# Kernel optimization log

Measured on AMD Instinct MI355X. Metric: run time of the kernel, lower is better.

Reference implementation:

```python
import jax, jax.numpy as jnp
import numpy as np

HID, NH, HD, MD = 512, 8, 64, 16  # hidden_dim, num_heads, head_dim, manifold_dim
B, S = 4, 1024
FLOW_STEPS, DT = 10, 0.1
EPS = 1e-8


def _cplx_weight(k, shape, std=0.02):
    kr, ki = jax.random.split(k)
    w = jax.random.normal(kr, shape) + 1j * jax.random.normal(ki, shape)
    return (w * std).astype(jnp.complex64)


def setup_inputs() -> dict:
    key = jax.random.key(0)
    ks = jax.random.split(key, 12)
    inp = {}
    inp['x_real'] = jax.random.normal(ks[0], (B, S, HID), dtype=jnp.float32)
    inp['x_imag'] = jax.random.normal(ks[1], (B, S, HID), dtype=jnp.float32)
    # manifold projection head_dim -> manifold_dim
    inp['Wm'] = _cplx_weight(ks[2], (MD, HD), std=HD ** -0.5)
    inp['bm'] = jnp.zeros((MD,), jnp.complex64)
    inp['Wq'] = _cplx_weight(ks[3], (MD, MD))
    inp['bq'] = jnp.zeros((MD,), jnp.complex64)
    inp['Wk'] = _cplx_weight(ks[4], (MD, MD))
    inp['bk'] = jnp.zeros((MD,), jnp.complex64)
    inp['Wv'] = _cplx_weight(ks[5], (MD, MD))
    inp['bv'] = jnp.zeros((MD,), jnp.complex64)
    # learned manifold metric (initialized to identity as in the module)
    inp['metric'] = jnp.eye(MD, dtype=jnp.complex64)
    # output projection expanded_dim = NH*MD -> hidden_dim
    inp['Wo'] = _cplx_weight(ks[6], (HID, NH * MD))
    inp['bo'] = jnp.zeros((HID,), jnp.complex64)
    return inp


def _forward(x_real, x_imag, Wm, bm, Wq, bq, Wk, bk, Wv, bv, metric, Wo, bo):
    x = (x_real + 1j * x_imag).astype(jnp.complex64)            # [B,S,HID]
    b, s, _ = x.shape
    h = x.reshape(b, s, NH, HD).transpose(0, 2, 1, 3)           # [B,NH,S,HD]
    # project onto low-dim manifold coordinates
    m = h @ Wm.T + bm                                           # [B,NH,S,MD]
    # hyperbolic exponential map at origin (curvature -1): tanh(|v|)/|v| * v
    n = jnp.sqrt(jnp.sum(jnp.abs(m) ** 2, -1, keepdims=True)) + EPS
    m = (jnp.tanh(n) / n) * m
    # parallel transport via the learned metric
    m = m @ metric
    # geometric flow: 10 Euler integration steps with dt=0.1
    sym = 0.5 * (metric + metric.conj().T)

    def step(carry, _):
        vel = carry @ sym - carry
        return carry + DT * vel, None

    m, _ = jax.lax.scan(step, m, None, length=FLOW_STEPS)
    # hyperbolic logarithm map at origin: artanh(|u|)/|u| * u
    n2 = jnp.sqrt(jnp.sum(jnp.abs(m) ** 2, -1, keepdims=True))
    n2 = jnp.clip(n2, EPS, 1.0 - 1e-6)
    m = (jnp.arctanh(n2) / n2) * m
    # complex q/k/v attention on manifold coordinates
    q = m @ Wq.T + bq
    k = m @ Wk.T + bk
    v = m @ Wv.T + bv
    scale = HD ** -0.5  # module uses self.scale = head_dim ** -0.5
    scores = jnp.einsum('bhsd,bhtd->bhst', q, jnp.conj(k)).real * scale  # [B,NH,S,S]
    attn = jax.nn.softmax(scores, axis=-1).astype(jnp.complex64)
    out = jnp.einsum('bhst,bhtd->bhsd', attn, v)                # [B,NH,S,MD]
    expanded = out.transpose(0, 2, 1, 3).reshape(b, s, NH * MD)  # [B,S,NH*MD]
    return expanded @ Wo.T + bo + x                              # residual, [B,S,HID]


def reference(x_real, x_imag, Wm, bm, Wq, bq, Wk, bk, Wv, bv, metric, Wo, bo):
    return _forward(x_real, x_imag, Wm, bm, Wq, bq, Wk, bk, Wv, bv, metric, Wo, bo)
```

## Files before the change

### kernel.cpp

```cpp
#include <hip/hip_runtime.h>
#include <math.h>

#define HIDD 512
#define NHH 8
#define HDD 64
#define MDD 16
#define Bz 4
#define Sz 1024
#define DTf 0.1f
#define EPSf 1e-8f
#define SCALEf 0.125f

typedef unsigned short ushort_t;
typedef unsigned int uint_t;

typedef __attribute__((ext_vector_type(8))) short bf16x8;
typedef __attribute__((ext_vector_type(4))) float f32x4;

constexpr size_t OFF_QB   = 0;
constexpr size_t OFF_KB   = OFF_QB + 262144;
constexpr size_t OFF_VT   = OFF_KB + 262144;
constexpr size_t OFF_E    = OFF_VT + 262144;
constexpr size_t OFF_WOT  = OFF_E + (size_t)Bz * Sz * NHH * MDD;

__device__ __forceinline__ float bf2f(ushort_t u) {
  union { unsigned int i; float f; } c;
  c.i = ((unsigned int)u) << 16;
  return c.f;
}
__device__ __forceinline__ ushort_t f2bf(float f) {
  unsigned int x = __float_as_uint(f);
  unsigned int r = (x + 0x7fffu + ((x >> 16) & 1u)) >> 16;
  return (ushort_t)r;
}
__device__ __forceinline__ float2 ldc(const void* p, int i, bool bf) {
  if (bf) {
    ushort2 u = ((const ushort2*)p)[i];
    return make_float2(bf2f(u.x), bf2f(u.y));
  }
  return ((const float2*)p)[i];
}
__device__ __forceinline__ float ldr(const void* p, size_t i, bool bf) {
  if (bf) return bf2f(((const ushort_t*)p)[i]);
  return ((const float*)p)[i];
}
__device__ __forceinline__ float2 cmadd(float2 acc, float2 a, float2 b) {
  acc.x = fmaf(a.x, b.x, fmaf(-a.y, b.y, acc.x));
  acc.y = fmaf(a.x, b.y, fmaf(a.y, b.x, acc.y));
  return acc;
}

__global__ __launch_bounds__(256) void k_qkv(
    const void* __restrict__ xr, const void* __restrict__ xi,
    const void* __restrict__ Wm, const void* __restrict__ bm,
    const void* __restrict__ Wq, const void* __restrict__ bq,
    const void* __restrict__ Wk, const void* __restrict__ bk,
    const void* __restrict__ Wv, const void* __restrict__ bv,
    const void* __restrict__ metric,
    ushort_t* __restrict__ Qb, ushort_t* __restrict__ Kb,
    ushort_t* __restrict__ VTb) {
  __shared__ float2 hs[64 * 65];
  __shared__ float2 msc[64 * 17];
  __shared__ float2 wmt[64 * 16];
  __shared__ float2 Tm[256];
  __shared__ float2 wqt[256], wkt[256], wvt[256];
  __shared__ float2 bms[16], bqs[16], bks[16], bvs[16];
  __shared__ int votes[4];
  float2* msc2 = hs;

  int tid = threadIdx.x;
  int bh = blockIdx.y;
  int s0 = blockIdx.x * 64;

  const uint_t* mu = (const uint_t*)metric;
  bool cbf = (mu[0] == 0x00003F80u);
  int ti = tid >> 4, tj = tid & 15;

  {
    unsigned e = (((const ushort_t*)xr)[tid] >> 7) & 0xFFu;
    unsigned long long bal = __ballot(e >= 100u && e <= 134u);
    if ((tid & 63) == 0) votes[tid >> 6] = (int)__popcll(bal);
  }

  wqt[tid] = ldc(metric, tid, cbf);
  #pragma unroll
  for (int it = 0; it < 4; it++) {
    int c = tid + it * 256;
    int d = c >> 6, e = c & 63;
    wmt[e * 16 + d] = ldc(Wm, c, cbf);
  }
  float2 wq_r = ldc(Wq, tid, cbf);
  float2 wk_r = ldc(Wk, tid, cbf);
  float2 wv_r = ldc(Wv, tid, cbf);
  float2 bm_r = make_float2(0.f, 0.f), bq_r = bm_r, bk_r = bm_r, bv_r = bm_r;
  if (tid < 16) {
    bm_r = ldc(bm, tid, cbf); bq_r = ldc(bq, tid, cbf);
    bk_r = ldc(bk, tid, cbf); bv_r = ldc(bv, tid, cbf);
  }
  __syncthreads();
  bool xbf = (votes[0] + votes[1] + votes[2] + votes[3]) > 192;

  size_t xoff = ((size_t)(((bh >> 3) * Sz) + s0)) * HIDD + (bh & 7) * HDD;
  ushort4 xur[4], xui[4];
  float4 xfr[4], xfi[4];
  if (xbf) {
    const ushort_t* xrb = (const ushort_t*)xr + xoff;
    const ushort_t* xib = (const ushort_t*)xi + xoff;
    #pragma unroll
    for (int it = 0; it < 4; it++) {
      int idx = tid + it * 256;
      int i = idx >> 4, e4 = idx & 15;
      xur[it] = ((const ushort4*)(xrb + (size_t)i * HIDD))[e4];
      xui[it] = ((const ushort4*)(xib + (size_t)i * HIDD))[e4];
    }
  } else {
    const float* xrb = (const float*)xr + xoff;
    const float* xib = (const float*)xi + xoff;
    #pragma unroll
    for (int it = 0; it < 4; it++) {
      int idx = tid + it * 256;
      int i = idx >> 4, e4 = idx & 15;
      xfr[it] = ((const float4*)(xrb + (size_t)i * HIDD))[e4];
      xfi[it] = ((const float4*)(xib + (size_t)i * HIDD))[e4];
    }
  }

  #define MATMUL16(DST, S1, S2)                                              \
    {                                                                        \
      float2 acc_ = make_float2(0.f, 0.f);                                   \
      _Pragma("unroll")                                                      \
      for (int k_ = 0; k_ < 16; k_++)                                        \
        acc_ = cmadd(acc_, S1[ti * 16 + k_], S2[k_ * 16 + tj]);              \
      DST[tid] = acc_;                                                       \
    }
  {
    float2 a = wqt[tid];
    float2 bt = wqt[tj * 16 + ti];
    float2 symv = make_float2(0.5f * (a.x + bt.x), 0.5f * (a.y - bt.y));
    float2 Mv = make_float2(DTf * symv.x, DTf * symv.y);
    if (ti == tj) Mv.x += 1.0f - DTf;
    wkt[tid] = Mv;
  }
  __syncthreads();
  MATMUL16(wvt, wkt, wkt);
  __syncthreads();
  MATMUL16(Tm, wvt, wvt);
  __syncthreads();
  MATMUL16(wvt, Tm, wkt);
  __syncthreads();
  MATMUL16(Tm, wvt, wvt);
  __syncthreads();
  float2 Tacc = make_float2(0.f, 0.f);
  #pragma unroll
  for (int k = 0; k < 16; k++) Tacc = cmadd(Tacc, wqt[ti * 16 + k], Tm[k * 16 + tj]);
  __syncthreads();
  #undef MATMUL16

  Tm[tid] = Tacc;
  wqt[tj * 16 + ti] = wq_r;
  wkt[tj * 16 + ti] = wk_r;
  wvt[tj * 16 + ti] = wv_r;
  if (tid < 16) { bms[tid] = bm_r; bqs[tid] = bq_r; bks[tid] = bk_r; bvs[tid] = bv_r; }
  if (xbf) {
    #pragma unroll
    for (int it = 0; it < 4; it++) {
      int idx = tid + it * 256;
      int i = idx >> 4, e = (idx & 15) * 4;
      hs[i * 65 + e + 0] = make_float2(bf2f(xur[it].x), bf2f(xui[it].x));
      hs[i * 65 + e + 1] = make_float2(bf2f(xur[it].y), bf2f(xui[it].y));
      hs[i * 65 + e + 2] = make_float2(bf2f(xur[it].z), bf2f(xui[it].z));
      hs[i * 65 + e + 3] = make_float2(bf2f(xur[it].w), bf2f(xui[it].w));
    }
  } else {
    #pragma unroll
    for (int it = 0; it < 4; it++) {
      int idx = tid + it * 256;
      int i = idx >> 4, e = (idx & 15) * 4;
      hs[i * 65 + e + 0] = make_float2(xfr[it].x, xfi[it].x);
      hs[i * 65 + e + 1] = make_float2(xfr[it].y, xfi[it].y);
      hs[i * 65 + e + 2] = make_float2(xfr[it].z, xfi[it].z);
      hs[i * 65 + e + 3] = make_float2(xfr[it].w, xfi[it].w);
    }
  }
  __syncthreads();

  int tok = tid >> 2, g = tid & 3;
  int jb = g * 4;

  float2 acc[4];
  #pragma unroll
  for (int i2 = 0; i2 < 4; i2++) acc[i2] = bms[jb + i2];
  for (int e = 0; e < 64; e++) {
    float2 hv = hs[tok * 65 + e];
    #pragma unroll
    for (int i2 = 0; i2 < 4; i2++) acc[i2] = cmadd(acc[i2], hv, wmt[e * 16 + jb + i2]);
  }
  float nn = 0.f;
  #pragma unroll
  for (int i2 = 0; i2 < 4; i2++) nn += acc[i2].x * acc[i2].x + acc[i2].y * acc[i2].y;
  nn += __shfl_xor(nn, 1);
  nn += __shfl_xor(nn, 2);
  float n1 = sqrtf(nn) + EPSf;
  float te = __expf(2.f * n1);
  float sc1 = (te - 1.f) / ((te + 1.f) * n1);
  #pragma unroll
  for (int i2 = 0; i2 < 4; i2++)
    msc[tok * 17 + jb + i2] = make_float2(acc[i2].x * sc1, acc[i2].y * sc1);
  __syncthreads();

  float2 m2[4];
  #pragma unroll
  for (int i2 = 0; i2 < 4; i2++) m2[i2] = make_float2(0.f, 0.f);
  for (int d = 0; d < 16; d++) {
    float2 mv = msc[tok * 17 + d];
    #pragma unroll
    for (int i2 = 0; i2 < 4; i2++) m2[i2] = cmadd(m2[i2], mv, Tm[d * 16 + jb + i2]);
  }
  float nn2 = 0.f;
  #pragma unroll
  for (int i2 = 0; i2 < 4; i2++) nn2 += m2[i2].x * m2[i2].x + m2[i2].y * m2[i2].y;
  nn2 += __shfl_xor(nn2, 1);
  nn2 += __shfl_xor(nn2, 2);
  float n2 = sqrtf(nn2);
  n2 = fminf(fmaxf(n2, EPSf), 1.0f - 1e-6f);
  float fac = 0.5f * __logf((1.f + n2) / (1.f - n2)) / n2;
  #pragma unroll
  for (int i2 = 0; i2 < 4; i2++)
    msc2[tok * 17 + jb + i2] = make_float2(m2[i2].x * fac, m2[i2].y * fac);
  __syncthreads();

  float2 qa[4], ka[4], va[4];
  #pragma unroll
  for (int i2 = 0; i2 < 4; i2++) { qa[i2] = bqs[jb + i2]; ka[i2] = bks[jb + i2]; va[i2] = bvs[jb + i2]; }
  for (int d = 0; d < 16; d++) {
    float2 mv = msc2[tok * 17 + d];
    #pragma unroll
    for (int i2 = 0; i2 < 4; i2++) {
      qa[i2] = cmadd(qa[i2], mv, wqt[d * 16 + jb + i2]);
      ka[i2] = cmadd(ka[i2], mv, wkt[d * 16 + jb + i2]);
      va[i2] = cmadd(va[i2], mv, wvt[d * 16 + jb + i2]);
    }
  }
  int s = s0 + tok;
  uint_t qp[4], kp[4];
  #pragma unroll
  for (int i2 = 0; i2 < 4; i2++) {
    qp[i2] = (uint_t)f2bf(qa[i2].x * SCALEf) | ((uint_t)f2bf(qa[i2].y * SCALEf) << 16);
    kp[i2] = (uint_t)f2bf(ka[i2].x) | ((uint_t)f2bf(ka[i2].y) << 16);
  }
  size_t rowbase = ((size_t)bh * Sz + s) * 32 + (size_t)g * 8;
  *(uint4*)(Qb + rowbase) = make_uint4(qp[0], qp[1], qp[2], qp[3]);
  *(uint4*)(Kb + rowbase) = make_uint4(kp[0], kp[1], kp[2], kp[3]);
  size_t vtb = (size_t)bh * 32 * Sz;
  #pragma unroll
  for (int i2 = 0; i2 < 4; i2++) {
    int d = (jb + i2) * 2;
    VTb[vtb + (size_t)d * Sz + s]       = f2bf(va[i2].x);
    VTb[vtb + (size_t)(d + 1) * Sz + s] = f2bf(va[i2].y);
  }
}

__global__ __launch_bounds__(256) void k_attn_mf(const ushort_t* __restrict__ Qb,
                                                 const ushort_t* __restrict__ Kb,
                                                 const ushort_t* __restrict__ VTb,
                                                 float* __restrict__ ef,
                                                 const void* __restrict__ Wo,
                                                 float2* __restrict__ WoT,
                                                 ushort_t* __restrict__ Ab,
                                                 ushort_t* __restrict__ Bb,
                                                 const void* __restrict__ metric,
                                                 int cmode) {
  __shared__ ushort_t Ks[128 * 88];
  __shared__ ushort_t VTs[32 * 152];
  __shared__ ushort_t Ps[4 * 16 * 136];
  int tid = threadIdx.x;

  {
    bool cbf = (((const uint_t*)metric)[0] == 0x00003F80u);
    if (tid < 128) {
      int idx = (blockIdx.y * 16 + blockIdx.x) * 128 + tid;
      float2 wv = ldc(Wo, idx, cbf);
      if (cmode) {
        int o = idx >> 7, j = idx & 127;
        WoT[(size_t)j * 512 + o] = wv;
      } else {
        ((ushort2*)Bb)[idx] = make_ushort2(f2bf(wv.x), f2bf(-wv.y));
      }
    }
  }

  int w = tid >> 6, lane = tid & 63;
  int n = lane & 15, qd = lane >> 4;
  int bh = blockIdx.y;
  int qb = blockIdx.x * 64 + w * 16;

  const ushort_t* Qh = Qb + (size_t)bh * Sz * 32;
  const ushort_t* Kh = Kb + (size_t)bh * Sz * 32;
  const ushort_t* VTh = VTb + (size_t)bh * 32 * Sz;

  bf16x8 qf = *(const bf16x8*)(Qh + (size_t)(qb + n) * 32 + qd * 8);

  f32x4 o0 = {0.f, 0.f, 0.f, 0.f}, o1 = {0.f, 0.f, 0.f, 0.f};
  float m_run = 0.f, l_run = 0.f;
  ushort_t* Pw = Ps + w * 16 * 136;

  for (int kc = 0; kc < Sz; kc += 128) {
    __syncthreads();
    {
      int row = tid >> 1, half = tid & 1;
      const uint4* sk = (const uint4*)(Kh + (size_t)(kc + row) * 32 + half * 16);
      uint4 a = sk[0], b2 = sk[1];
      *(uint4*)(Ks + row * 88 + half * 16) = a;
      *(uint4*)(Ks + row * 88 + half * 16 + 8) = b2;
      int d = tid >> 3, seg = tid & 7;
      const uint4* sv = (const uint4*)(VTh + (size_t)d * Sz + kc + seg * 16);
      uint4 c = sv[0], e2 = sv[1];
      *(uint4*)(VTs + d * 152 + seg * 16) = c;
      *(uint4*)(VTs + d * 152 + seg * 16 + 8) = e2;
    }
    __syncthreads();

    f32x4 st[8];
    __builtin_amdgcn_s_setprio(1);
    #pragma unroll
    for (int s = 0; s < 4; s++) {
      bf16x8 ka0 = *(const bf16x8*)(Ks + (s * 32 + n) * 88 + qd * 8);
      bf16x8 ka1 = *(const bf16x8*)(Ks + (s * 32 + 16 + n) * 88 + qd * 8);
      f32x4 z = {0.f, 0.f, 0.f, 0.f};
      st[2 * s]     = __builtin_amdgcn_mfma_f32_16x16x32_bf16(ka0, qf, z, 0, 0, 0);
      st[2 * s + 1] = __builtin_amdgcn_mfma_f32_16x16x32_bf16(ka1, qf, z, 0, 0, 0);
    }
    __builtin_amdgcn_s_setprio(0);

    float mt = st[0][0];
    #pragma unroll
    for (int i = 0; i < 8; i++) {
      #pragma unroll
      for (int r = 0; r < 4; r++) mt = fmaxf(mt, st[i][r]);
    }
    mt = fmaxf(mt, __shfl_xor(mt, 16));
    mt = fmaxf(mt, __shfl_xor(mt, 32));
    if (!__all(mt - m_run <= 8.f)) {
      float mnew = fmaxf(m_run, mt);
      float alpha = __expf(m_run - mnew);
      l_run *= alpha;
      float ar0 = __shfl(alpha, qd * 4 + 0);
      float ar1 = __shfl(alpha, qd * 4 + 1);
      float ar2 = __shfl(alpha, qd * 4 + 2);
      float ar3 = __shfl(alpha, qd * 4 + 3);
      o0[0] *= ar0; o0[1] *= ar1; o0[2] *= ar2; o0[3] *= ar3;
      o1[0] *= ar0; o1[1] *= ar1; o1[2] *= ar2; o1[3] *= ar3;
      m_run = mnew;
    }

    float lt = 0.f;
    #pragma unroll
    for (int s = 0; s < 4; s++) {
      float p0[4], p1[4];
      #pragma unroll
      for (int r = 0; r < 4; r++) {
        p0[r] = __expf(st[2 * s][r] - m_run);
        p1[r] = __expf(st[2 * s + 1][r] - m_run);
        lt += p0[r] + p1[r];
      }
      uint2 w0, w1;
      w0.x = (uint_t)f2bf(p0[0]) | ((uint_t)f2bf(p0[1]) << 16);
      w0.y = (uint_t)f2bf(p0[2]) | ((uint_t)f2bf(p0[3]) << 16);
      w1.x = (uint_t)f2bf(p1[0]) | ((uint_t)f2bf(p1[1]) << 16);
      w1.y = (uint_t)f2bf(p1[2]) | ((uint_t)f2bf(p1[3]) << 16);
      *(uint2*)(Pw + n * 136 + s * 32 + qd * 4) = w0;
      *(uint2*)(Pw + n * 136 + s * 32 + 16 + qd * 4) = w1;
    }
    l_run += lt;

    __builtin_amdgcn_s_setprio(1);
    #pragma unroll
    for (int s = 0; s < 4; s++) {
      bf16x8 pa  = *(const bf16x8*)(Pw + n * 136 + s * 32 + qd * 8);
      bf16x8 vb0 = *(const bf16x8*)(VTs + n * 152 + s * 32 + qd * 8);
      bf16x8 vb1 = *(const bf16x8*)(VTs + (n + 16) * 152 + s * 32 + qd * 8);
      o0 = __builtin_amdgcn_mfma_f32_16x16x32_bf16(pa, vb0, o0, 0, 0, 0);
      o1 = __builtin_amdgcn_mfma_f32_16x16x32_bf16(pa, vb1, o1, 0, 0, 0);
    }
    __builtin_amdgcn_s_setprio(0);
  }

  l_run += __shfl_xor(l_run, 16);
  l_run += __shfl_xor(l_run, 32);
  int b = bh >> 3, h = bh & 7;
  if (cmode == 0) {
    #pragma unroll
    for (int r = 0; r < 4; r++) {
      float li = __shfl(l_run, qd * 4 + r);
      float inv = 1.0f / li;
      size_t gt = (size_t)(b * Sz + qb + qd * 4 + r);
      Ab[gt * 256 + h * 32 + n]      = f2bf(o0[r] * inv);
      Ab[gt * 256 + h * 32 + 16 + n] = f2bf(o1[r] * inv);
    }
  } else {
    #pragma unroll
    for (int r = 0; r < 4; r++) {
      float li = __shfl(l_run, qd * 4 + r);
      float inv = 1.0f / li;
      int tok = qb + qd * 4 + r;
      float* ep = ef + (((size_t)(b * Sz + tok)) * NHH + h) * 32;
      ep[n]      = o0[r] * inv;
      ep[16 + n] = o1[r] * inv;
    }
  }
}

__global__ __launch_bounds__(256) void k_proj_mf(const ushort_t* __restrict__ Ab,
                                                 const ushort_t* __restrict__ Bb,
                                                 const void* __restrict__ bo,
                                                 const void* __restrict__ xr,
                                                 const void* __restrict__ metric,
                                                 float* __restrict__ out) {
  __shared__ int votes[4];
  int tid = threadIdx.x;
  bool cbf = (((const uint_t*)metric)[0] == 0x00003F80u);
  {
    unsigned e = (((const ushort_t*)xr)[tid] >> 7) & 0xFFu;
    unsigned long long bal = __ballot(e >= 100u && e <= 134u);
    if ((tid & 63) == 0) votes[tid >> 6] = (int)__popcll(bal);
  }
  __syncthreads();
  bool xbf = (votes[0] + votes[1] + votes[2] + votes[3]) > 192;

  int w = tid >> 6, lane = tid & 63;
  int n = lane & 15, qd = lane >> 4;
  int tb = blockIdx.x * 16;
  int ob = blockIdx.y * 256 + w * 64;

  bf16x8 af[8];
  const ushort_t* Ar = Ab + (size_t)(tb + n) * 256 + qd * 8;
  #pragma unroll
  for (int ks = 0; ks < 8; ks++) af[ks] = *(const bf16x8*)(Ar + ks * 32);

  #pragma unroll
  for (int nt = 0; nt < 4; nt++) {
    int o = ob + nt * 16 + n;
    const ushort_t* Br = Bb + (size_t)o * 256 + qd * 8;
    f32x4 c = {0.f, 0.f, 0.f, 0.f};
    #pragma unroll
    for (int ks = 0; ks < 8; ks++) {
      bf16x8 bfr = *(const bf16x8*)(Br + ks * 32);
      c = __builtin_amdgcn_mfma_f32_16x16x32_bf16(bfr, af[ks], c, 0, 0, 0);
    }
    float bor = ldc(bo, o, cbf).x;
    #pragma unroll
    for (int r = 0; r < 4; r++) {
      size_t gt = (size_t)(tb + qd * 4 + r);
      out[gt * HIDD + o] = c[r] + bor + ldr(xr, gt * HIDD + o, xbf);
    }
  }
}

__global__ __launch_bounds__(256) void k_proj_c(const float2* __restrict__ ew,
                                                const float2* __restrict__ WoT,
                                                const void* __restrict__ bo,
                                                const void* __restrict__ xr,
                                                const void* __restrict__ xi,
                                                const void* __restrict__ metric,
                                                ushort2* __restrict__ out) {
  __shared__ float2 es[8 * 128];
  __shared__ int votes[4];
  int tid = threadIdx.x;
  bool cbf = (((const uint_t*)metric)[0] == 0x00003F80u);
  {
    unsigned e = (((const ushort_t*)xr)[tid] >> 7) & 0xFFu;
    unsigned long long bal = __ballot(e >= 100u && e <= 134u);
    if ((tid & 63) == 0) votes[tid >> 6] = (int)__popcll(bal);
  }
  int tok0 = blockIdx.x * 8;
  #pragma unroll
  for (int it = 0; it < 4; it++) {
    int idx = tid + it * 256;
    es[idx] = ew[(size_t)tok0 * 128 + idx];
  }
  __syncthreads();
  bool xbf = (votes[0] + votes[1] + votes[2] + votes[3]) > 192;
  for (int rep = 0; rep < 2; rep++) {
    int o = tid + rep * 256;
    float2 accT[8];
    #pragma unroll
    for (int t = 0; t < 8; t++) accT[t] = make_float2(0.f, 0.f);
    #pragma unroll 2
    for (int j = 0; j < 128; j++) {
      float2 wv = WoT[(size_t)j * 512 + o];
      #pragma unroll
      for (int t = 0; t < 8; t++) accT[t] = cmadd(accT[t], es[t * 128 + j], wv);
    }
    float2 bov = ldc(bo, o, cbf);
    #pragma unroll
    for (int t = 0; t < 8; t++) {
      size_t gt = tok0 + t;
      float rx = accT[t].x + bov.x + ldr(xr, gt * HIDD + o, xbf);
      float ry = accT[t].y + bov.y + ldr(xi, gt * HIDD + o, xbf);
      out[gt * HIDD + o] = make_ushort2(f2bf(ry), f2bf(rx));
    }
  }
}

extern "C" void kernel_launch(void* const* d_in, const int* in_sizes, int n_in,
                              void* d_out, int out_size, void* d_ws, size_t ws_size,
                              hipStream_t stream) {
  const void* xr     = d_in[0];
  const void* xi     = d_in[1];
  const void* Wm     = d_in[2];
  const void* bm     = d_in[3];
  const void* Wq     = d_in[4];
  const void* bq     = d_in[5];
  const void* Wk     = d_in[6];
  const void* bk     = d_in[7];
  const void* Wv     = d_in[8];
  const void* bv     = d_in[9];
  const void* metric = d_in[10];
  const void* Wo     = d_in[11];
  const void* bo     = d_in[12];

  float2* W = (float2*)d_ws;
  ushort_t* Qb  = (ushort_t*)(W + OFF_QB);
  ushort_t* Kb  = (ushort_t*)(W + OFF_KB);
  ushort_t* VTb = (ushort_t*)(W + OFF_VT);
  ushort_t* Ab  = (ushort_t*)(W + OFF_E);
  ushort_t* Bb  = (ushort_t*)(W + OFF_WOT);

  int cmode = (out_size == Bz * Sz * HIDD) ? 0 : 1;

  k_qkv<<<dim3(16, 32), 256, 0, stream>>>(xr, xi, Wm, bm, Wq, bq, Wk, bk, Wv, bv,
                                          metric, Qb, Kb, VTb);
  k_attn_mf<<<dim3(16, 32), 256, 0, stream>>>(Qb, Kb, VTb, (float*)(W + OFF_E),
                                              Wo, W + OFF_WOT, Ab, Bb, metric, cmode);
  if (cmode == 0) {
    k_proj_mf<<<dim3(256, 2), 256, 0, stream>>>(Ab, Bb, bo, xr, metric,
                                                (float*)d_out);
  } else {
    k_proj_c<<<512, 256, 0, stream>>>(W + OFF_E, W + OFF_WOT, bo, xr, xi, metric,
                                      (ushort2*)d_out);
  }
}
```

Baseline: 136.1 us.

## Vectorize QKV smem reads, prefetch K/V tiles, use exp2 and packed bf16 conversion

The QKV kernel pads its shared arrays to even strides so it can read operands with 16-byte loads and unroll its loops. The attention kernel now loads the next K/V tile from global memory into registers while computing on the current tile. Softmax uses the hardware exp2 with log2(e) folded into the Q scale, and bf16 packing uses the packed conversion intrinsic. The prefetch raises register pressure, and the wider LDS reads may change bank-conflict behaviour.

```diff
diff --git a/kernel.cpp b/kernel.cpp
--- a/kernel.cpp
+++ b/kernel.cpp
@@ -1,4 +1,5 @@
 #include <hip/hip_runtime.h>
+#include <hip/hip_bf16.h>
 #include <math.h>
 
 #define HIDD 512
@@ -10,6 +11,7 @@
 #define DTf 0.1f
 #define EPSf 1e-8f
 #define SCALEf 0.125f
+#define QSCALEf 0.18033688f
 
 typedef unsigned short ushort_t;
 typedef unsigned int uint_t;
@@ -32,6 +34,11 @@
   unsigned int x = __float_as_uint(f);
   unsigned int r = (x + 0x7fffu + ((x >> 16) & 1u)) >> 16;
   return (ushort_t)r;
+}
+__device__ __forceinline__ uint_t pkbf(float a, float b) {
+  union { __hip_bfloat162 h; uint_t u; } c;
+  c.h = __float22bfloat162_rn(make_float2(a, b));
+  return c.u;
 }
 __device__ __forceinline__ float2 ldc(const void* p, int i, bool bf) {
   if (bf) {
@@ -59,11 +66,11 @@
     const void* __restrict__ metric,
     ushort_t* __restrict__ Qb, ushort_t* __restrict__ Kb,
     ushort_t* __restrict__ VTb) {
-  __shared__ float2 hs[64 * 65];
-  __shared__ float2 msc[64 * 17];
-  __shared__ float2 wmt[64 * 16];
-  __shared__ float2 Tm[256];
-  __shared__ float2 wqt[256], wkt[256], wvt[256];
+  __shared__ __align__(16) float2 hs[64 * 66];
+  __shared__ __align__(16) float2 msc[64 * 18];
+  __shared__ __align__(16) float2 wmt[64 * 16];
+  __shared__ __align__(16) float2 Tm[256];
+  __shared__ __align__(16) float2 wqt[256], wkt[256], wvt[256];
   __shared__ float2 bms[16], bqs[16], bks[16], bvs[16];
   __shared__ int votes[4];
   float2* msc2 = hs;
@@ -166,20 +173,20 @@
     for (int it = 0; it < 4; it++) {
       int idx = tid + it * 256;
       int i = idx >> 4, e = (idx & 15) * 4;
-      hs[i * 65 + e + 0] = make_float2(bf2f(xur[it].x), bf2f(xui[it].x));
-      hs[i * 65 + e + 1] = make_float2(bf2f(xur[it].y), bf2f(xui[it].y));
-      hs[i * 65 + e + 2] = make_float2(bf2f(xur[it].z), bf2f(xui[it].z));
-      hs[i * 65 + e + 3] = make_float2(bf2f(xur[it].w), bf2f(xui[it].w));
+      hs[i * 66 + e + 0] = make_float2(bf2f(xur[it].x), bf2f(xui[it].x));
+      hs[i * 66 + e + 1] = make_float2(bf2f(xur[it].y), bf2f(xui[it].y));
+      hs[i * 66 + e + 2] = make_float2(bf2f(xur[it].z), bf2f(xui[it].z));
+      hs[i * 66 + e + 3] = make_float2(bf2f(xur[it].w), bf2f(xui[it].w));
     }
   } else {
     #pragma unroll
     for (int it = 0; it < 4; it++) {
       int idx = tid + it * 256;
       int i = idx >> 4, e = (idx & 15) * 4;
-      hs[i * 65 + e + 0] = make_float2(xfr[it].x, xfi[it].x);
-      hs[i * 65 + e + 1] = make_float2(xfr[it].y, xfi[it].y);
-      hs[i * 65 + e + 2] = make_float2(xfr[it].z, xfi[it].z);
-      hs[i * 65 + e + 3] = make_float2(xfr[it].w, xfi[it].w);
+      hs[i * 66 + e + 0] = make_float2(xfr[it].x, xfi[it].x);
+      hs[i * 66 + e + 1] = make_float2(xfr[it].y, xfi[it].y);
+      hs[i * 66 + e + 2] = make_float2(xfr[it].z, xfi[it].z);
+      hs[i * 66 + e + 3] = make_float2(xfr[it].w, xfi[it].w);
     }
   }
   __syncthreads();
@@ -190,10 +197,22 @@
   float2 acc[4];
   #pragma unroll
   for (int i2 = 0; i2 < 4; i2++) acc[i2] = bms[jb + i2];
-  for (int e = 0; e < 64; e++) {
-    float2 hv = hs[tok * 65 + e];
-    #pragma unroll
-    for (int i2 = 0; i2 < 4; i2++) acc[i2] = cmadd(acc[i2], hv, wmt[e * 16 + jb + i2]);
+  #pragma unroll 4
+  for (int e = 0; e < 64; e += 2) {
+    float4 hv2 = *(const float4*)(&hs[tok * 66 + e]);
+    float2 hv0 = make_float2(hv2.x, hv2.y), hv1 = make_float2(hv2.z, hv2.w);
+    float4 wa0 = *(const float4*)(&wmt[e * 16 + jb]);
+    float4 wb0 = *(const float4*)(&wmt[e * 16 + jb + 2]);
+    float4 wa1 = *(const float4*)(&wmt[(e + 1) * 16 + jb]);
+    float4 wb1 = *(const float4*)(&wmt[(e + 1) * 16 + jb + 2]);
+    acc[0] = cmadd(acc[0], hv0, make_float2(wa0.x, wa0.y));
+    acc[1] = cmadd(acc[1], hv0, make_float2(wa0.z, wa0.w));
+    acc[2] = cmadd(acc[2], hv0, make_float2(wb0.x, wb0.y));
+    acc[3] = cmadd(acc[3], hv0, make_float2(wb0.z, wb0.w));
+    acc[0] = cmadd(acc[0], hv1, make_float2(wa1.x, wa1.y));
+    acc[1] = cmadd(acc[1], hv1, make_float2(wa1.z, wa1.w));
+    acc[2] = cmadd(acc[2], hv1, make_float2(wb1.x, wb1.y));
+    acc[3] = cmadd(acc[3], hv1, make_float2(wb1.z, wb1.w));
   }
   float nn = 0.f;
   #pragma unroll
@@ -203,18 +222,31 @@
   float n1 = sqrtf(nn) + EPSf;
   float te = __expf(2.f * n1);
   float sc1 = (te - 1.f) / ((te + 1.f) * n1);
-  #pragma unroll
-  for (int i2 = 0; i2 < 4; i2++)
-    msc[tok * 17 + jb + i2] = make_float2(acc[i2].x * sc1, acc[i2].y * sc1);
+  *(float4*)(&msc[tok * 18 + jb]) =
+      make_float4(acc[0].x * sc1, acc[0].y * sc1, acc[1].x * sc1, acc[1].y * sc1);
+  *(float4*)(&msc[tok * 18 + jb + 2]) =
+      make_float4(acc[2].x * sc1, acc[2].y * sc1, acc[3].x * sc1, acc[3].y * sc1);
   __syncthreads();
 
   float2 m2[4];
   #pragma unroll
   for (int i2 = 0; i2 < 4; i2++) m2[i2] = make_float2(0.f, 0.f);
-  for (int d = 0; d < 16; d++) {
-    float2 mv = msc[tok * 17 + d];
-    #pragma unroll
-    for (int i2 = 0; i2 < 4; i2++) m2[i2] = cmadd(m2[i2], mv, Tm[d * 16 + jb + i2]);
+  #pragma unroll
+  for (int d = 0; d < 16; d += 2) {
+    float4 mvv = *(const float4*)(&msc[tok * 18 + d]);
+    float2 mv0 = make_float2(mvv.x, mvv.y), mv1 = make_float2(mvv.z, mvv.w);
+    float4 t0a = *(const float4*)(&Tm[d * 16 + jb]);
+    float4 t0b = *(const float4*)(&Tm[d * 16 + jb + 2]);
+    float4 t1a = *(const float4*)(&Tm[(d + 1) * 16 + jb]);
+    float4 t1b = *(const float4*)(&Tm[(d + 1) * 16 + jb + 2]);
+    m2[0] = cmadd(m2[0], mv0, make_float2(t0a.x, t0a.y));
+    m2[1] = cmadd(m2[1], mv0, make_float2(t0a.z, t0a.w));
+    m2[2] = cmadd(m2[2], mv0, make_float2(t0b.x, t0b.y));
+    m2[3] = cmadd(m2[3], mv0, make_float2(t0b.z, t0b.w));
+    m2[0] = cmadd(m2[0], mv1, make_float2(t1a.x, t1a.y));
+    m2[1] = cmadd(m2[1], mv1, make_float2(t1a.z, t1a.w));
+    m2[2] = cmadd(m2[2], mv1, make_float2(t1b.x, t1b.y));
+    m2[3] = cmadd(m2[3], mv1, make_float2(t1b.z, t1b.w));
   }
   float nn2 = 0.f;
   #pragma unroll
@@ -224,29 +256,49 @@
   float n2 = sqrtf(nn2);
   n2 = fminf(fmaxf(n2, EPSf), 1.0f - 1e-6f);
   float fac = 0.5f * __logf((1.f + n2) / (1.f - n2)) / n2;
-  #pragma unroll
-  for (int i2 = 0; i2 < 4; i2++)
-    msc2[tok * 17 + jb + i2] = make_float2(m2[i2].x * fac, m2[i2].y * fac);
+  *(float4*)(&msc2[tok * 18 + jb]) =
+      make_float4(m2[0].x * fac, m2[0].y * fac, m2[1].x * fac, m2[1].y * fac);
+  *(float4*)(&msc2[tok * 18 + jb + 2]) =
+      make_float4(m2[2].x * fac, m2[2].y * fac, m2[3].x * fac, m2[3].y * fac);
   __syncthreads();
 
   float2 qa[4], ka[4], va[4];
   #pragma unroll
   for (int i2 = 0; i2 < 4; i2++) { qa[i2] = bqs[jb + i2]; ka[i2] = bks[jb + i2]; va[i2] = bvs[jb + i2]; }
-  for (int d = 0; d < 16; d++) {
-    float2 mv = msc2[tok * 17 + d];
-    #pragma unroll
-    for (int i2 = 0; i2 < 4; i2++) {
-      qa[i2] = cmadd(qa[i2], mv, wqt[d * 16 + jb + i2]);
-      ka[i2] = cmadd(ka[i2], mv, wkt[d * 16 + jb + i2]);
-      va[i2] = cmadd(va[i2], mv, wvt[d * 16 + jb + i2]);
+  #pragma unroll
+  for (int d = 0; d < 16; d += 2) {
+    float4 mvv = *(const float4*)(&msc2[tok * 18 + d]);
+    float2 mv0 = make_float2(mvv.x, mvv.y), mv1 = make_float2(mvv.z, mvv.w);
+    #pragma unroll
+    for (int half = 0; half < 2; half++) {
+      int dd = d + half;
+      float2 mv = half ? mv1 : mv0;
+      float4 qA = *(const float4*)(&wqt[dd * 16 + jb]);
+      float4 qB = *(const float4*)(&wqt[dd * 16 + jb + 2]);
+      float4 kA = *(const float4*)(&wkt[dd * 16 + jb]);
+      float4 kB = *(const float4*)(&wkt[dd * 16 + jb + 2]);
+      float4 vA = *(const float4*)(&wvt[dd * 16 + jb]);
+      float4 vB = *(const float4*)(&wvt[dd * 16 + jb + 2]);
+      qa[0] = cmadd(qa[0], mv, make_float2(qA.x, qA.y));
+      qa[1] = cmadd(qa[1], mv, make_float2(qA.z, qA.w));
+      qa[2] = cmadd(qa[2], mv, make_float2(qB.x, qB.y));
+      qa[3] = cmadd(qa[3], mv, make_float2(qB.z, qB.w));
+      ka[0] = cmadd(ka[0], mv, make_float2(kA.x, kA.y));
+      ka[1] = cmadd(ka[1], mv, make_float2(kA.z, kA.w));
+      ka[2] = cmadd(ka[2], mv, make_float2(kB.x, kB.y));
+      ka[3] = cmadd(ka[3], mv, make_float2(kB.z, kB.w));
+      va[0] = cmadd(va[0], mv, make_float2(vA.x, vA.y));
+      va[1] = cmadd(va[1], mv, make_float2(vA.z, vA.w));
+      va[2] = cmadd(va[2], mv, make_float2(vB.x, vB.y));
+      va[3] = cmadd(va[3], mv, make_float2(vB.z, vB.w));
     }
   }
   int s = s0 + tok;
   uint_t qp[4], kp[4];
   #pragma unroll
   for (int i2 = 0; i2 < 4; i2++) {
-    qp[i2] = (uint_t)f2bf(qa[i2].x * SCALEf) | ((uint_t)f2bf(qa[i2].y * SCALEf) << 16);
-    kp[i2] = (uint_t)f2bf(ka[i2].x) | ((uint_t)f2bf(ka[i2].y) << 16);
+    qp[i2] = pkbf(qa[i2].x * QSCALEf, qa[i2].y * QSCALEf);
+    kp[i2] = pkbf(ka[i2].x, ka[i2].y);
   }
   size_t rowbase = ((size_t)bh * Sz + s) * 32 + (size_t)g * 8;
   *(uint4*)(Qb + rowbase) = make_uint4(qp[0], qp[1], qp[2], qp[3]);
@@ -284,7 +336,7 @@
         int o = idx >> 7, j = idx & 127;
         WoT[(size_t)j * 512 + o] = wv;
       } else {
-        ((ushort2*)Bb)[idx] = make_ushort2(f2bf(wv.x), f2bf(-wv.y));
+        ((uint_t*)Bb)[idx] = pkbf(wv.x, -wv.y);
       }
     }
   }
@@ -304,21 +356,29 @@
   float m_run = 0.f, l_run = 0.f;
   ushort_t* Pw = Ps + w * 16 * 136;
 
+  int row = tid >> 1, half = tid & 1;
+  int vd = tid >> 3, seg = tid & 7;
+  uint4 kA, kB, vA, vB;
+  {
+    const uint4* sk = (const uint4*)(Kh + (size_t)row * 32 + half * 16);
+    kA = sk[0]; kB = sk[1];
+    const uint4* sv = (const uint4*)(VTh + (size_t)vd * Sz + seg * 16);
+    vA = sv[0]; vB = sv[1];
+  }
+
   for (int kc = 0; kc < Sz; kc += 128) {
     __syncthreads();
-    {
-      int row = tid >> 1, half = tid & 1;
-      const uint4* sk = (const uint4*)(Kh + (size_t)(kc + row) * 32 + half * 16);
-      uint4 a = sk[0], b2 = sk[1];
-      *(uint4*)(Ks + row * 88 + half * 16) = a;
-      *(uint4*)(Ks + row * 88 + half * 16 + 8) = b2;
-      int d = tid >> 3, seg = tid & 7;
-      const uint4* sv = (const uint4*)(VTh + (size_t)d * Sz + kc + seg * 16);
-      uint4 c = sv[0], e2 = sv[1];
-      *(uint4*)(VTs + d * 152 + seg * 16) = c;
-      *(uint4*)(VTs + d * 152 + seg * 16 + 8) = e2;
-    }
+    *(uint4*)(Ks + row * 88 + half * 16)     = kA;
+    *(uint4*)(Ks + row * 88 + half * 16 + 8) = kB;
+    *(uint4*)(VTs + vd * 152 + seg * 16)     = vA;
+    *(uint4*)(VTs + vd * 152 + seg * 16 + 8) = vB;
     __syncthreads();
+    if (kc + 128 < Sz) {
+      const uint4* sk = (const uint4*)(Kh + (size_t)(kc + 128 + row) * 32 + half * 16);
+      kA = sk[0]; kB = sk[1];
+      const uint4* sv = (const uint4*)(VTh + (size_t)vd * Sz + (kc + 128) + seg * 16);
+      vA = sv[0]; vB = sv[1];
+    }
 
     f32x4 st[8];
     __builtin_amdgcn_s_setprio(1);
@@ -332,17 +392,17 @@
     }
     __builtin_amdgcn_s_setprio(0);
 
-    float mt = st[0][0];
-    #pragma unroll
-    for (int i = 0; i < 8; i++) {
-      #pragma unroll
-      for (int r = 0; r < 4; r++) mt = fmaxf(mt, st[i][r]);
-    }
+    float m4[8];
+    #pragma unroll
+    for (int i = 0; i < 8; i++)
+      m4[i] = fmaxf(fmaxf(st[i][0], st[i][1]), fmaxf(st[i][2], st[i][3]));
+    float mt = fmaxf(fmaxf(fmaxf(m4[0], m4[1]), fmaxf(m4[2], m4[3])),
+                     fmaxf(fmaxf(m4[4], m4[5]), fmaxf(m4[6], m4[7])));
     mt = fmaxf(mt, __shfl_xor(mt, 16));
     mt = fmaxf(mt, __shfl_xor(mt, 32));
     if (!__all(mt - m_run <= 8.f)) {
       float mnew = fmaxf(m_run, mt);
-      float alpha = __expf(m_run - mnew);
+      float alpha = __builtin_amdgcn_exp2f(m_run - mnew);
       l_run *= alpha;
       float ar0 = __shfl(alpha, qd * 4 + 0);
       float ar1 = __shfl(alpha, qd * 4 + 1);
@@ -359,15 +419,15 @@
       float p0[4], p1[4];
       #pragma unroll
       for (int r = 0; r < 4; r++) {
-        p0[r] = __expf(st[2 * s][r] - m_run);
-        p1[r] = __expf(st[2 * s + 1][r] - m_run);
+        p0[r] = __builtin_amdgcn_exp2f(st[2 * s][r] - m_run);
+        p1[r] = __builtin_amdgcn_exp2f(st[2 * s + 1][r] - m_run);
         lt += p0[r] + p1[r];
       }
       uint2 w0, w1;
-      w0.x = (uint_t)f2bf(p0[0]) | ((uint_t)f2bf(p0[1]) << 16);
-      w0.y = (uint_t)f2bf(p0[2]) | ((uint_t)f2bf(p0[3]) << 16);
-      w1.x = (uint_t)f2bf(p1[0]) | ((uint_t)f2bf(p1[1]) << 16);
-      w1.y = (uint_t)f2bf(p1[2]) | ((uint_t)f2bf(p1[3]) << 16);
+      w0.x = pkbf(p0[0], p0[1]);
+      w0.y = pkbf(p0[2], p0[3]);
+      w1.x = pkbf(p1[0], p1[1]);
+      w1.y = pkbf(p1[2], p1[3]);
       *(uint2*)(Pw + n * 136 + s * 32 + qd * 4) = w0;
       *(uint2*)(Pw + n * 136 + s * 32 + 16 + qd * 4) = w1;
     }
```

New measurement: 133.6 us. No clear change (-1.9%).
